# Kernel optimization log

Hardware: AMD Instinct MI355X
Metric: run time of the kernel (lower is better)

## Reference

```python
import jax, jax.numpy as jnp
import numpy as np

IN_CAPS = 8      # I
IN_DIM = 768     # E (== D here, required by the module's reshape/matmul)
NUM_CAPS = 8     # J
DIM_CAPS = 768   # D
NUM_ROUTING = 3
EPS = 1e-8

def _pearsonr(x, y):
    # correlation along the last (capsule) dim, keepdims -> [..., 1]
    xm = x - jnp.mean(x, axis=-1, keepdims=True)
    ym = y - jnp.mean(y, axis=-1, keepdims=True)
    num = jnp.sum(xm * ym, axis=-1, keepdims=True)
    den = jnp.sqrt(jnp.sum(xm * xm, axis=-1, keepdims=True) * jnp.sum(ym * ym, axis=-1, keepdims=True))
    return num / (den + EPS)

def _squash(s):
    n2 = jnp.sum(s * s, axis=-1, keepdims=True)
    return (n2 / (1.0 + n2)) * s / jnp.sqrt(n2 + EPS)

def setup_inputs() -> dict:
    key = jax.random.key(0)
    k1, k2, k3, k4, k5 = jax.random.split(key, 5)
    m = jax.random.normal(k1, (IN_CAPS, IN_DIM), dtype=jnp.float32)
    q = jax.random.normal(k2, (400, IN_DIM), dtype=jnp.float32)
    # W built from a shared seed expanded over in_caps, as in the torch module
    W_share = 0.01 * jax.random.normal(k3, (1, NUM_CAPS, 1, DIM_CAPS, IN_DIM), dtype=jnp.float32)
    W = jnp.broadcast_to(W_share, (1, NUM_CAPS, IN_CAPS, DIM_CAPS, IN_DIM)).copy()
    b = jnp.ones((1, NUM_CAPS, IN_CAPS, DIM_CAPS), dtype=jnp.float32)
    W_n = jax.random.normal(k4, (IN_DIM, DIM_CAPS), dtype=jnp.float32)
    return {"m": m, "q": q, "W": W, "b": b, "W_n": W_n}

def reference(m, q, W, b, W_n):
    Wj = W[0]  # [J, I, D, E]
    N = q.shape[0]
    # memory projection: [I, E] @ [E, D] -> [I, D] (D == E)
    m_proj = m @ W_n
    # hat_m_ij: [1, J, I, D]
    hat_m = jnp.einsum('jide,ie->jid', Wj, m_proj)[None] + b
    # hat_q_ij: [N, J, I, D]
    hat_q = jnp.einsum('jide,ne->njid', Wj, q)
    tmp_m = jax.lax.stop_gradient(hat_m)
    tmp_q = jax.lax.stop_gradient(hat_q)
    a = jnp.zeros((N, NUM_CAPS, IN_CAPS, 1), dtype=q.dtype)
    p = jnp.tanh(_pearsonr(tmp_m, tmp_q))  # [N, J, I, 1]
    for _ in range(NUM_ROUTING - 1):
        d = jax.nn.softmax(a, axis=1)                      # over capsules J
        hat_v = jnp.sum((d + p) * tmp_m, axis=2)           # [N, J, D]
        v = _squash(hat_v)                                 # [N, J, D]
        cos = jnp.einsum('jid,njd->nji', tmp_m[0], v)[..., None]  # [N, J, I, 1]
        a = a + tmp_q * cos                                # broadcasts to [N, J, I, D]
        tmp_q = 0.5 * (tmp_q + v[:, :, None, :])
        p = jnp.tanh(_pearsonr(tmp_m, tmp_q))
    d = jax.nn.softmax(a, axis=1)
    hat_v = jnp.sum((d + p) * hat_m, axis=2)               # grads flow through hat_m here
    v_out = _squash(hat_v)                                 # [N, J, D]
    return v_out.reshape(N, -1)                            # [N, J*D]
```

## Files before the change

### kernel.cpp

```cpp
#include <hip/hip_runtime.h>
#include <math.h>

#define DD    768
#define NQ    400
#define NROWS 408
#define JD    6144
#define WSLICE 4718592
#define EPSF  1e-8f
#define K2    2304
#define K2S   1536

#define OFF_H     0
#define OFF_HM    (OFF_H + 408*6144)
#define OFF_MU    (OFF_HM + 64*768)
#define OFF_MC2   (OFF_MU + 64)
#define OFF_G     (OFF_MC2 + 64)
#define OFF_DMQ   (OFF_G + 512)
#define OFF_SQ0   (OFF_DMQ + 400*64)
#define OFF_SQ20  (OFF_SQ0 + 400*8)
#define OFF_A2    (OFF_SQ20 + 400*8)
#define OFF_B2    (OFF_A2 + 512*K2S/2)

#define FOR8(M) M(0) M(1) M(2) M(3) M(4) M(5) M(6) M(7)

typedef __attribute__((ext_vector_type(8))) short short8v;
typedef __attribute__((ext_vector_type(4))) float float4v;

__device__ inline unsigned short f2bf(float x) {
    unsigned u = __float_as_uint(x);
    u += 0x7FFF + ((u >> 16) & 1);
    return (unsigned short)(u >> 16);
}
__device__ inline float bf2f(unsigned short h) {
    return __uint_as_float(((unsigned)h) << 16);
}

__global__ __launch_bounds__(256) void k_cvt(const float* __restrict__ q,
                                             const float* __restrict__ m,
                                             const float* __restrict__ Wn,
                                             const float* __restrict__ W,
                                             unsigned short* __restrict__ A2,
                                             unsigned short* __restrict__ B2)
{
    const int bid = blockIdx.x;
    const int tid = threadIdx.x;
    if (bid < 408) {
        const int r = bid;
        unsigned short* dst = A2 + (size_t)r * K2S;
        if (r < NQ) {
            const float* src = q + (size_t)r * DD;
            #pragma unroll
            for (int u0 = 0; u0 < 3; ++u0) {
                const int u = u0 * 256 + tid;
                float x = src[u];
                unsigned short hi = f2bf(x);
                unsigned short lo = f2bf(x - bf2f(hi));
                dst[u] = hi; dst[DD + u] = lo;
            }
        } else {
            const int i = r - NQ;
            float a0 = 0.f, a1 = 0.f, a2 = 0.f;
            #pragma unroll 8
            for (int e = 0; e < DD; ++e) {
                const float mv = m[i*DD + e];
                const float* wr = Wn + (size_t)e * DD;
                a0 += mv * wr[tid];
                a1 += mv * wr[tid + 256];
                a2 += mv * wr[tid + 512];
            }
            #pragma unroll
            for (int u0 = 0; u0 < 3; ++u0) {
                const int u = u0 * 256 + tid;
                float x = (u0 == 0) ? a0 : (u0 == 1) ? a1 : a2;
                unsigned short hi = f2bf(x);
                unsigned short lo = f2bf(x - bf2f(hi));
                dst[u] = hi; dst[DD + u] = lo;
            }
        }
    } else {
        const int r0 = (bid - 408) * 4;
        #pragma unroll
        for (int rr = 0; rr < 4; ++rr) {
            const int rw = r0 + rr;
            const int jj = rw / 768;
            const int d  = rw - jj * 768;
            const float* src = W + (size_t)jj * WSLICE + (size_t)d * DD;
            unsigned short* dst = B2 + (size_t)rw * K2S;
            #pragma unroll
            for (int u0 = 0; u0 < 3; ++u0) {
                const int u = u0 * 256 + tid;
                float x = src[u];
                unsigned short hi = f2bf(x);
                unsigned short lo = f2bf(x - bf2f(hi));
                dst[u] = hi; dst[DD + u] = lo;
            }
        }
    }
}

__global__ __launch_bounds__(256) void k_gemm_mfma(const unsigned short* __restrict__ A2,
                                                   const unsigned short* __restrict__ B2,
                                                   float* __restrict__ H)
{
    __shared__ __align__(16) unsigned short lds[2][12288];
    const int tid = threadIdx.x;
    const int wv  = tid >> 6;
    const int ln  = tid & 63;
    const int c0  = blockIdx.x * 64;
    const int m0  = blockIdx.y * 128;
    const int wm  = (wv >> 1) * 64;
    const int wn  = (wv & 1) * 32;
    const unsigned short* Ap = A2 + (size_t)m0 * K2S;
    const unsigned short* Bp = B2 + (size_t)c0 * K2S;

    float4v acc[4][2];
    #pragma unroll
    for (int a = 0; a < 4; ++a)
        #pragma unroll
        for (int b = 0; b < 2; ++b)
            acc[a][b] = (float4v){0.f, 0.f, 0.f, 0.f};

#define STAGE(buf, ka, kb) {                                                      \
    _Pragma("unroll")                                                             \
    for (int qq = 0; qq < 4; ++qq) {                                              \
        const int idx = (qq << 8) + tid;                             \
        const int row = idx >> 3;                                     \
        const int ce  = ((idx & 7) ^ (row & 7)) << 3;                             \
        __builtin_amdgcn_global_load_lds(                                         \
            (const __attribute__((address_space(1))) void*)(Ap + (size_t)row * K2S + (ka) + ce), \
            (__attribute__((address_space(3))) void*)(&lds[buf][idx * 8]), 16, 0, 0);            \
    }                                                                             \
    _Pragma("unroll")                                                             \
    for (int qq = 0; qq < 2; ++qq) {                                              \
        const int idx = (qq << 8) + tid;                              \
        const int row = idx >> 3;                                      \
        const int ce  = ((idx & 7) ^ (row & 7)) << 3;                             \
        __builtin_amdgcn_global_load_lds(                                         \
            (const __attribute__((address_space(1))) void*)(Bp + (size_t)row * K2S + (kb) + ce), \
            (__attribute__((address_space(3))) void*)(&lds[buf][8192 + idx * 8]), 16, 0, 0);     \
    } }

#define COMPUTE(buf) { _Pragma("unroll")                                          \
    for (int s = 0; s < 2; ++s) {                                                 \
        short8v af[4], bf[2];                                                     \
        _Pragma("unroll")                                                         \
        for (int mi = 0; mi < 4; ++mi) {                                          \
            const int row = wm + mi * 16 + (ln & 15);                             \
            const int off = row * 64 + ((s * 32 + ((ln >> 4) * 8)) ^ ((row & 7) << 3)); \
            af[mi] = *reinterpret_cast<const short8v*>(&lds[buf][off]);           \
        }                                                                         \
        _Pragma("unroll")                                                         \
        for (int ni = 0; ni < 2; ++ni) {                                          \
            const int row = wn + ni * 16 + (ln & 15);                             \
            const int off = row * 64 + ((s * 32 + ((ln >> 4) * 8)) ^ ((row & 7) << 3)); \
            bf[ni] = *reinterpret_cast<const short8v*>(&lds[buf][8192 + off]);    \
        }                                                                         \
        _Pragma("unroll")                                                         \
        for (int mi = 0; mi < 4; ++mi)                                            \
            _Pragma("unroll")                                                     \
            for (int ni = 0; ni < 2; ++ni)                                        \
                acc[mi][ni] = __builtin_amdgcn_mfma_f32_16x16x32_bf16(af[mi], bf[ni], acc[mi][ni], 0, 0, 0); \
    } }

    STAGE(0, 0, 0);
    __syncthreads();
    int cur = 0;
    for (int k0 = 64; k0 < K2; k0 += 64) {
        const int ka = (k0 < 1536) ? k0 : k0 - 1536;
        const int kb = (k0 < 768)  ? k0 : k0 - 768;
        STAGE(cur ^ 1, ka, kb);
        COMPUTE(cur);
        __syncthreads();
        cur ^= 1;
    }
    COMPUTE(cur);
#undef STAGE
#undef COMPUTE

    #pragma unroll
    for (int mi = 0; mi < 4; ++mi) {
        #pragma unroll
        for (int r = 0; r < 4; ++r) {
            const int gr = m0 + wm + mi * 16 + (ln >> 4) * 4 + r;
            if (gr < NROWS) {
                #pragma unroll
                for (int ni = 0; ni < 2; ++ni)
                    H[(size_t)gr * JD + c0 + wn + ni * 16 + (ln & 15)] = acc[mi][ni][r];
            }
        }
    }
}

__global__ __launch_bounds__(256) void k_mid(const float* __restrict__ H,
                                             const float* __restrict__ b,
                                             float* __restrict__ hm,
                                             float* __restrict__ muM,
                                             float* __restrict__ mc2M,
                                             float* __restrict__ G,
                                             float* __restrict__ dmq,
                                             float* __restrict__ Sq0v,
                                             float* __restrict__ Sq20v)
{
    const int bid = blockIdx.x;
    const int tid = threadIdx.x;
    const int lane = tid & 63, wave = tid >> 6;
    __shared__ __align__(16) float Ms[8][768];
    __shared__ float scr[8][4];
    __shared__ float smu;

    if (bid < 64) {
        const int ji = bid;
        const int j = ji >> 3, i = ji & 7;
        float vals[3];
        float s = 0.f;
        #pragma unroll
        for (int u = 0; u < 3; ++u) {
            const int d = u * 256 + tid;
            float x = H[(size_t)(NQ + i) * JD + j * DD + d] + b[(size_t)ji * DD + d];
            hm[(size_t)ji * DD + d] = x;
            vals[u] = x;
            s += x;
        }
        #pragma unroll
        for (int off = 32; off; off >>= 1) s += __shfl_down(s, off);
        if (lane == 0) scr[0][wave] = s;
        __syncthreads();
        if (tid == 0) smu = (scr[0][0] + scr[0][1] + scr[0][2] + scr[0][3]) * (1.f / 768.f);
        __syncthreads();
        const float mu = smu;
        float s2 = 0.f;
        #pragma unroll
        for (int u = 0; u < 3; ++u) { float c = vals[u] - mu; s2 += c * c; }
        __syncthreads();
        #pragma unroll
        for (int off = 32; off; off >>= 1) s2 += __shfl_down(s2, off);
        if (lane == 0) scr[0][wave] = s2;
        __syncthreads();
        if (tid == 0) { muM[ji] = mu; mc2M[ji] = scr[0][0] + scr[0][1] + scr[0][2] + scr[0][3]; }
    } else if (bid < 128) {
        const int ji = bid - 64;
        const int j = ji >> 3, i = ji & 7;
        const float* Hj = H + j * DD;
        const float* bj = b + (size_t)(j * 8) * DD;
        const float a0 = Hj[(size_t)(NQ + i) * JD + tid]       + bj[(size_t)i * DD + tid];
        const float a1 = Hj[(size_t)(NQ + i) * JD + 256 + tid] + bj[(size_t)i * DD + 256 + tid];
        const float a2 = Hj[(size_t)(NQ + i) * JD + 512 + tid] + bj[(size_t)i * DD + 512 + tid];
#define GDOT(k) { const float* Hp = Hj + (size_t)(NQ + k) * JD + tid;            \
        const float* bp = bj + (size_t)k * DD + tid;                             \
        float acc = a0*(Hp[0]+bp[0]) + a1*(Hp[256]+bp[256]) + a2*(Hp[512]+bp[512]); \
        acc += __shfl_down(acc, 32); acc += __shfl_down(acc, 16);                \
        acc += __shfl_down(acc, 8);  acc += __shfl_down(acc, 4);                 \
        acc += __shfl_down(acc, 2);  acc += __shfl_down(acc, 1);                 \
        if (lane == 0) scr[k][wave] = acc; }
        FOR8(GDOT)
#undef GDOT
        __syncthreads();
        if (tid < 8) G[ji*8 + tid] = scr[tid][0] + scr[tid][1] + scr[tid][2] + scr[tid][3];
    } else {
        const int t = bid - 128;
        const int j = t & 7;
        const int tile = t >> 3;
        #pragma unroll
        for (int r = 0; r < 8; ++r)
            for (int c = tid; c < DD; c += 256)
                Ms[r][c] = H[(size_t)(NQ + r) * JD + j * DD + c] + b[(size_t)(j * 8 + r) * DD + c];
        __syncthreads();

        for (int nn = wave; nn < 25; nn += 4) {
            const int n = tile * 25 + nn;
            const float* qp = H + (size_t)n * JD + j * DD;
            float s = 0.f, s2 = 0.f;
#define DCL(k) float d##k = 0.f;
            FOR8(DCL)
#undef DCL
            #pragma unroll 2
            for (int c = 0; c < 12; ++c) {
                const int d = lane + 64 * c;
                const float qv = qp[d];
                s += qv; s2 += qv * qv;
#define MAC(k) d##k += qv * Ms[k][d];
                FOR8(MAC)
#undef MAC
            }
#define XR(v) { v += __shfl_xor(v, 32); v += __shfl_xor(v, 16); v += __shfl_xor(v, 8); \
                v += __shfl_xor(v, 4);  v += __shfl_xor(v, 2);  v += __shfl_xor(v, 1); }
#define XRD(k) XR(d##k)
            FOR8(XRD)
#undef XRD
            XR(s) XR(s2)
#undef XR
            if (lane == 0) {
#define ST(k) dmq[(size_t)n*64 + j*8 + k] = d##k;
                FOR8(ST)
#undef ST
                Sq0v[n*8 + j] = s;
                Sq20v[n*8 + j] = s2;
            }
        }
    }
}

__global__ __launch_bounds__(768) void k_route2(const float* __restrict__ H,
                                                const float* __restrict__ hm,
                                                const float* __restrict__ muM,
                                                const float* __restrict__ mc2M,
                                                const float* __restrict__ G,
                                                const float* __restrict__ dmq,
                                                const float* __restrict__ Sq0v,
                                                const float* __restrict__ Sq20v,
                                                float* __restrict__ out)
{
    const int n = blockIdx.x;
    const int tid = threadIdx.x;
    const int lane = tid & 63, wave = tid >> 6;
    __shared__ __align__(16) float sVv[8][768];
    __shared__ float scr[24][12];
    __shared__ float rstat[24];
    __shared__ float sDot[64];
    __shared__ float sP[64], sC1[64], sC2[64], sB1[64];

#define WRED(val, idx) { float _v = (val);                           \
    _v += __shfl_down(_v, 32); _v += __shfl_down(_v, 16);            \
    _v += __shfl_down(_v, 8);  _v += __shfl_down(_v, 4);             \
    _v += __shfl_down(_v, 2);  _v += __shfl_down(_v, 1);             \
    if (lane == 0) scr[(idx)][wave] = _v; }

#define FIN(nv) { if (tid < (nv)) { float _s = 0.f;                  \
    _Pragma("unroll")                                                \
    for (int _w = 0; _w < 12; ++_w) _s += scr[tid][_w];              \
    rstat[tid] = _s; } }

#define DOTLOOP() for (int t = wave; t < 64; t += 12) {              \
        const int _j = t >> 3;                                       \
        const float* Mrow = hm + (size_t)t * DD;                     \
        float acc = 0.f;                                             \
        _Pragma("unroll")                                            \
        for (int c = 0; c < 3; ++c) {                                \
            const int dd = c * 256 + lane * 4;                       \
            const float4 mv = *reinterpret_cast<const float4*>(Mrow + dd);       \
            const float4 vv = *reinterpret_cast<const float4*>(&sVv[_j][dd]);    \
            acc += mv.x*vv.x + mv.y*vv.y + mv.z*vv.z + mv.w*vv.w;    \
        }                                                            \
        acc += __shfl_down(acc, 32); acc += __shfl_down(acc, 16);    \
        acc += __shfl_down(acc, 8);  acc += __shfl_down(acc, 4);     \
        acc += __shfl_down(acc, 2);  acc += __shfl_down(acc, 1);     \
        if (lane == 0) sDot[t] = acc;                                \
    }

#define XR3(v) { v += __shfl_xor(v, 1); v += __shfl_xor(v, 2); v += __shfl_xor(v, 4); }

    float w0 = 0.f, s1 = 0.f, dotM1 = 0.f, Sq1 = 0.f, Sq21 = 0.f, mu = 0.f, mc2 = 0.f;
    if (tid < 64) {
        const int j = lane >> 3;
        mu  = muM[lane];
        mc2 = mc2M[lane];
        const float smR = 768.f * mu;
        const float dq  = dmq[(size_t)n * 64 + lane];
        const float Sq  = Sq0v[n * 8 + j];
        const float Sq2v = Sq20v[n * 8 + j];
        {
            float num  = dq - mu * Sq;
            float varq = fmaxf(Sq2v - Sq * Sq * (1.f / 768.f), 0.f);
            float den  = sqrtf(mc2 * varq) + EPSF;
            w0 = tanhf(num / den) + 0.125f;
        }
        const float* Gr = G + lane * 8;
        const int base = lane & ~7;
        float gw = 0.f;
        #pragma unroll
        for (int ii = 0; ii < 8; ++ii) gw += Gr[ii] * __shfl(w0, base + ii);
        float n2h1 = w0 * gw;  XR3(n2h1);
        float dqh1 = w0 * dq;  XR3(dqh1);
        float Sh1  = w0 * smR; XR3(Sh1);
        s1 = n2h1 / ((1.f + n2h1) * sqrtf(n2h1 + EPSF));
        float c1 = s1 * gw;
        sC1[lane] = c1;
        sB1[lane] = 0.5f * s1 * w0;
        dotM1 = 0.5f * (dq + c1);
        Sq1   = 0.5f * (Sq + s1 * Sh1);
        Sq21  = 0.25f * (Sq2v + 2.f * s1 * dqh1 + s1 * s1 * n2h1);
        float varq1 = fmaxf(Sq21 - Sq1 * Sq1 * (1.f / 768.f), 0.f);
        sP[lane] = tanhf((dotM1 - mu * Sq1) / (sqrtf(mc2 * varq1) + EPSF));
    }
    __syncthreads();

    const float* Hn = H + (size_t)n * JD + tid;
    const float* hmp = hm + tid;
#define DECL(k) float t0_##k = Hn[k * DD]; float tq1_##k = 0.5f * t0_##k; float vh_##k = 0.f;
    FOR8(DECL)
#undef DECL
    #pragma unroll 2
    for (int i = 0; i < 8; ++i) {
#define XA(k) float x##k = t0_##k * sC1[k * 8 + i];
        FOR8(XA)
#undef XA
        float mx = fmaxf(fmaxf(fmaxf(x0, x1), fmaxf(x2, x3)),
                         fmaxf(fmaxf(x4, x5), fmaxf(x6, x7)));
#define XE(k) x##k = __expf(x##k - mx);
        FOR8(XE)
#undef XE
        float inv = 1.f / (x0 + x1 + x2 + x3 + x4 + x5 + x6 + x7);
#define XACC(k) { const float mval = hmp[(size_t)(k * 8 + i) * DD];  \
        vh_##k  += (x##k * inv + sP[k * 8 + i]) * mval;              \
        tq1_##k += sB1[k * 8 + i] * mval; }
        FOR8(XACC)
#undef XACC
    }
#define STG(k) sVv[k][tid] = vh_##k;                                 \
    WRED(vh_##k * vh_##k, k); WRED(vh_##k, 8 + k); WRED(t0_##k * vh_##k, 16 + k);
    FOR8(STG)
#undef STG
    __syncthreads();
    DOTLOOP();
    FIN(24);
    __syncthreads();

    if (tid < 64) {
        const int j = lane >> 3;
        const float n2h2 = rstat[j];
        const float Sh2  = rstat[8 + j];
        const float dqh2 = rstat[16 + j];
        const float u = sDot[lane];
        float s2 = n2h2 / ((1.f + n2h2) * sqrtf(n2h2 + EPSF));
        float c2 = s2 * u;
        sC2[lane] = c2;
        float dotM2 = 0.5f * (dotM1 + c2);
        float w0u = w0 * u; XR3(w0u);
        float dt1h2 = 0.5f * (dqh2 + s1 * w0u);
        float Sq2_ = 0.5f * (Sq1 + s2 * Sh2);
        float Sq22 = 0.25f * Sq21 + 0.5f * s2 * dt1h2 + 0.25f * s2 * s2 * n2h2;
        float varq2 = fmaxf(Sq22 - Sq2_ * Sq2_ * (1.f / 768.f), 0.f);
        sP[lane] = tanhf((dotM2 - mu * Sq2_) / (sqrtf(mc2 * varq2) + EPSF));
    }
    __syncthreads();

#define ZV(k) vh_##k = 0.f;
    FOR8(ZV)
#undef ZV
    #pragma unroll 2
    for (int i = 0; i < 8; ++i) {
#define XA(k) float x##k = t0_##k * sC1[k * 8 + i] + tq1_##k * sC2[k * 8 + i];
        FOR8(XA)
#undef XA
        float mx = fmaxf(fmaxf(fmaxf(x0, x1), fmaxf(x2, x3)),
                         fmaxf(fmaxf(x4, x5), fmaxf(x6, x7)));
#define XE(k) x##k = __expf(x##k - mx);
        FOR8(XE)
#undef XE
        float inv = 1.f / (x0 + x1 + x2 + x3 + x4 + x5 + x6 + x7);
#define XACC(k) vh_##k += (x##k * inv + sP[k * 8 + i]) * hmp[(size_t)(k * 8 + i) * DD];
        FOR8(XACC)
#undef XACC
    }
#define NRM(k) WRED(vh_##k * vh_##k, k);
    FOR8(NRM)
#undef NRM
    __syncthreads();
    FIN(8);
    __syncthreads();
    float* On = out + (size_t)n * JD + tid;
#define WOUT(k) { float n2 = rstat[k];                               \
        float sc = n2 / ((1.f + n2) * sqrtf(n2 + EPSF));             \
        On[k * DD] = vh_##k * sc; }
    FOR8(WOUT)
#undef WOUT
#undef WRED
#undef FIN
#undef DOTLOOP
#undef XR3
}

extern "C" void kernel_launch(void* const* d_in, const int* in_sizes, int n_in,
                              void* d_out, int out_size, void* d_ws, size_t ws_size,
                              hipStream_t stream) {
    const float* m  = (const float*)d_in[0];
    const float* q  = (const float*)d_in[1];
    const float* W  = (const float*)d_in[2];
    const float* b  = (const float*)d_in[3];
    const float* Wn = (const float*)d_in[4];
    float* out = (float*)d_out;
    float* ws  = (float*)d_ws;

    float* H     = ws + OFF_H;
    float* hm    = ws + OFF_HM;
    float* muM   = ws + OFF_MU;
    float* mc2M  = ws + OFF_MC2;
    float* G     = ws + OFF_G;
    float* dmq   = ws + OFF_DMQ;
    float* Sq0v  = ws + OFF_SQ0;
    float* Sq20v = ws + OFF_SQ20;
    unsigned short* A2 = (unsigned short*)(ws + OFF_A2);
    unsigned short* B2 = (unsigned short*)(ws + OFF_B2);

    k_cvt<<<dim3(1944), 256, 0, stream>>>(q, m, Wn, W, A2, B2);
    k_gemm_mfma<<<dim3(96, 4), 256, 0, stream>>>(A2, B2, H);
    k_mid<<<dim3(256), 256, 0, stream>>>(H, b, hm, muM, mc2M, G, dmq, Sq0v, Sq20v);
    k_route2<<<dim3(400), 768, 0, stream>>>(H, hm, muM, mc2M, G, dmq, Sq0v, Sq20v, out);
}
```

Measured before the change: 150.0 us.

## Fold per-query memory dot and sum statistics into routing kernel

Moves the per-query dot products against hat_m and the query sum and sum-of-squares out of k_mid and into k_route2. They are now computed from the t0 values each thread already holds, using shared-memory reductions, so the dmq/Sq0/Sq20 global buffers and their round-trip are removed and k_mid shrinks to 128 blocks. It also sets an occupancy hint of 3 on k_route2 and fully unrolls the two routing loops. The costs are extra reduction work and synchronisations in k_route2 and possible register pressure from the full unroll.

```diff
diff --git a/kernel.cpp b/kernel.cpp
--- a/kernel.cpp
+++ b/kernel.cpp
@@ -15,10 +15,7 @@
 #define OFF_MU    (OFF_HM + 64*768)
 #define OFF_MC2   (OFF_MU + 64)
 #define OFF_G     (OFF_MC2 + 64)
-#define OFF_DMQ   (OFF_G + 512)
-#define OFF_SQ0   (OFF_DMQ + 400*64)
-#define OFF_SQ20  (OFF_SQ0 + 400*8)
-#define OFF_A2    (OFF_SQ20 + 400*8)
+#define OFF_A2    (OFF_G + 512)
 #define OFF_B2    (OFF_A2 + 512*K2S/2)
 
 #define FOR8(M) M(0) M(1) M(2) M(3) M(4) M(5) M(6) M(7)
@@ -123,8 +120,8 @@
 #define STAGE(buf, ka, kb) {                                                      \
     _Pragma("unroll")                                                             \
     for (int qq = 0; qq < 4; ++qq) {                                              \
-        const int idx = (qq << 8) + tid;                             \
-        const int row = idx >> 3;                                     \
+        const int idx = (qq << 8) + tid;                                          \
+        const int row = idx >> 3;                                                 \
         const int ce  = ((idx & 7) ^ (row & 7)) << 3;                             \
         __builtin_amdgcn_global_load_lds(                                         \
             (const __attribute__((address_space(1))) void*)(Ap + (size_t)row * K2S + (ka) + ce), \
@@ -132,8 +129,8 @@
     }                                                                             \
     _Pragma("unroll")                                                             \
     for (int qq = 0; qq < 2; ++qq) {                                              \
-        const int idx = (qq << 8) + tid;                              \
-        const int row = idx >> 3;                                      \
+        const int idx = (qq << 8) + tid;                                          \
+        const int row = idx >> 3;                                                 \
         const int ce  = ((idx & 7) ^ (row & 7)) << 3;                             \
         __builtin_amdgcn_global_load_lds(                                         \
             (const __attribute__((address_space(1))) void*)(Bp + (size_t)row * K2S + (kb) + ce), \
@@ -196,15 +193,11 @@
                                              float* __restrict__ hm,
                                              float* __restrict__ muM,
                                              float* __restrict__ mc2M,
-                                             float* __restrict__ G,
-                                             float* __restrict__ dmq,
-                                             float* __restrict__ Sq0v,
-                                             float* __restrict__ Sq20v)
+                                             float* __restrict__ G)
 {
     const int bid = blockIdx.x;
     const int tid = threadIdx.x;
     const int lane = tid & 63, wave = tid >> 6;
-    __shared__ __align__(16) float Ms[8][768];
     __shared__ float scr[8][4];
     __shared__ float smu;
 
@@ -237,7 +230,7 @@
         if (lane == 0) scr[0][wave] = s2;
         __syncthreads();
         if (tid == 0) { muM[ji] = mu; mc2M[ji] = scr[0][0] + scr[0][1] + scr[0][2] + scr[0][3]; }
-    } else if (bid < 128) {
+    } else {
         const int ji = bid - 64;
         const int j = ji >> 3, i = ji & 7;
         const float* Hj = H + j * DD;
@@ -256,59 +249,15 @@
 #undef GDOT
         __syncthreads();
         if (tid < 8) G[ji*8 + tid] = scr[tid][0] + scr[tid][1] + scr[tid][2] + scr[tid][3];
-    } else {
-        const int t = bid - 128;
-        const int j = t & 7;
-        const int tile = t >> 3;
-        #pragma unroll
-        for (int r = 0; r < 8; ++r)
-            for (int c = tid; c < DD; c += 256)
-                Ms[r][c] = H[(size_t)(NQ + r) * JD + j * DD + c] + b[(size_t)(j * 8 + r) * DD + c];
-        __syncthreads();
-
-        for (int nn = wave; nn < 25; nn += 4) {
-            const int n = tile * 25 + nn;
-            const float* qp = H + (size_t)n * JD + j * DD;
-            float s = 0.f, s2 = 0.f;
-#define DCL(k) float d##k = 0.f;
-            FOR8(DCL)
-#undef DCL
-            #pragma unroll 2
-            for (int c = 0; c < 12; ++c) {
-                const int d = lane + 64 * c;
-                const float qv = qp[d];
-                s += qv; s2 += qv * qv;
-#define MAC(k) d##k += qv * Ms[k][d];
-                FOR8(MAC)
-#undef MAC
-            }
-#define XR(v) { v += __shfl_xor(v, 32); v += __shfl_xor(v, 16); v += __shfl_xor(v, 8); \
-                v += __shfl_xor(v, 4);  v += __shfl_xor(v, 2);  v += __shfl_xor(v, 1); }
-#define XRD(k) XR(d##k)
-            FOR8(XRD)
-#undef XRD
-            XR(s) XR(s2)
-#undef XR
-            if (lane == 0) {
-#define ST(k) dmq[(size_t)n*64 + j*8 + k] = d##k;
-                FOR8(ST)
-#undef ST
-                Sq0v[n*8 + j] = s;
-                Sq20v[n*8 + j] = s2;
-            }
-        }
-    }
-}
-
-__global__ __launch_bounds__(768) void k_route2(const float* __restrict__ H,
-                                                const float* __restrict__ hm,
-                                                const float* __restrict__ muM,
-                                                const float* __restrict__ mc2M,
-                                                const float* __restrict__ G,
-                                                const float* __restrict__ dmq,
-                                                const float* __restrict__ Sq0v,
-                                                const float* __restrict__ Sq20v,
-                                                float* __restrict__ out)
+    }
+}
+
+__global__ __launch_bounds__(768, 3) void k_route2(const float* __restrict__ H,
+                                                   const float* __restrict__ hm,
+                                                   const float* __restrict__ muM,
+                                                   const float* __restrict__ mc2M,
+                                                   const float* __restrict__ G,
+                                                   float* __restrict__ out)
 {
     const int n = blockIdx.x;
     const int tid = threadIdx.x;
@@ -349,15 +298,28 @@
 
 #define XR3(v) { v += __shfl_xor(v, 1); v += __shfl_xor(v, 2); v += __shfl_xor(v, 4); }
 
+    const float* Hn = H + (size_t)n * JD + tid;
+    const float* hmp = hm + tid;
+#define DECL(k) float t0_##k = Hn[k * DD]; sVv[k][tid] = t0_##k; float tq1_##k, vh_##k;
+    FOR8(DECL)
+#undef DECL
+#define STAT0(k) WRED(t0_##k, k); WRED(t0_##k * t0_##k, 8 + k);
+    FOR8(STAT0)
+#undef STAT0
+    __syncthreads();
+    DOTLOOP();
+    FIN(16);
+    __syncthreads();
+
     float w0 = 0.f, s1 = 0.f, dotM1 = 0.f, Sq1 = 0.f, Sq21 = 0.f, mu = 0.f, mc2 = 0.f;
     if (tid < 64) {
         const int j = lane >> 3;
         mu  = muM[lane];
         mc2 = mc2M[lane];
         const float smR = 768.f * mu;
-        const float dq  = dmq[(size_t)n * 64 + lane];
-        const float Sq  = Sq0v[n * 8 + j];
-        const float Sq2v = Sq20v[n * 8 + j];
+        const float dq  = sDot[lane];
+        const float Sq  = rstat[j];
+        const float Sq2v = rstat[8 + j];
         {
             float num  = dq - mu * Sq;
             float varq = fmaxf(Sq2v - Sq * Sq * (1.f / 768.f), 0.f);
@@ -384,12 +346,10 @@
     }
     __syncthreads();
 
-    const float* Hn = H + (size_t)n * JD + tid;
-    const float* hmp = hm + tid;
-#define DECL(k) float t0_##k = Hn[k * DD]; float tq1_##k = 0.5f * t0_##k; float vh_##k = 0.f;
-    FOR8(DECL)
-#undef DECL
-    #pragma unroll 2
+#define INIT1(k) tq1_##k = 0.5f * t0_##k; vh_##k = 0.f;
+    FOR8(INIT1)
+#undef INIT1
+    #pragma unroll
     for (int i = 0; i < 8; ++i) {
 #define XA(k) float x##k = t0_##k * sC1[k * 8 + i];
         FOR8(XA)
@@ -437,7 +397,7 @@
 #define ZV(k) vh_##k = 0.f;
     FOR8(ZV)
 #undef ZV
-    #pragma unroll 2
+    #pragma unroll
     for (int i = 0; i < 8; ++i) {
 #define XA(k) float x##k = t0_##k * sC1[k * 8 + i] + tq1_##k * sC2[k * 8 + i];
         FOR8(XA)
@@ -486,14 +446,11 @@
     float* muM   = ws + OFF_MU;
     float* mc2M  = ws + OFF_MC2;
     float* G     = ws + OFF_G;
-    float* dmq   = ws + OFF_DMQ;
-    float* Sq0v  = ws + OFF_SQ0;
-    float* Sq20v = ws + OFF_SQ20;
     unsigned short* A2 = (unsigned short*)(ws + OFF_A2);
     unsigned short* B2 = (unsigned short*)(ws + OFF_B2);
 
     k_cvt<<<dim3(1944), 256, 0, stream>>>(q, m, Wn, W, A2, B2);
     k_gemm_mfma<<<dim3(96, 4), 256, 0, stream>>>(A2, B2, H);
-    k_mid<<<dim3(256), 256, 0, stream>>>(H, b, hm, muM, mc2M, G, dmq, Sq0v, Sq20v);
-    k_route2<<<dim3(400), 768, 0, stream>>>(H, hm, muM, mc2M, G, dmq, Sq0v, Sq20v, out);
-}
+    k_mid<<<dim3(128), 256, 0, stream>>>(H, b, hm, muM, mc2M, G);
+    k_route2<<<dim3(400), 768, 0, stream>>>(H, hm, muM, mc2M, G, out);
+}
```

After: 263.8 us. 75.9% more time.
